# Performance work log

Hardware: AMD Instinct MI355X
Metric: run time of the kernel (lower is better)

Reference implementation:

```python
import jax, jax.numpy as jnp
import numpy as np

B, S, D_MODEL = 8, 1024, 1024
N_HEADS, N_KV_HEADS, HEAD_DIM = 16, 8, 64
ROPE_THETA = 10000.0
LN_EPS = 1e-12


def setup_inputs() -> dict:
    key = jax.random.key(0)
    ks = jax.random.split(key, 6)
    sc = 0.02
    return {
        "hidden_states": jax.random.normal(ks[0], (B, S, D_MODEL), jnp.float32),
        "Wq": jax.random.normal(ks[1], (D_MODEL, N_HEADS * HEAD_DIM), jnp.float32) * sc,
        "bq": jnp.zeros((N_HEADS * HEAD_DIM,), jnp.float32),
        "Wk": jax.random.normal(ks[2], (D_MODEL, N_KV_HEADS * HEAD_DIM), jnp.float32) * sc,
        "bk": jnp.zeros((N_KV_HEADS * HEAD_DIM,), jnp.float32),
        "Wv": jax.random.normal(ks[3], (D_MODEL, N_KV_HEADS * HEAD_DIM), jnp.float32) * sc,
        "bv": jnp.zeros((N_KV_HEADS * HEAD_DIM,), jnp.float32),
        "Wo": jax.random.normal(ks[4], (N_HEADS * HEAD_DIM, D_MODEL), jnp.float32) * sc,
        "bo": jnp.zeros((D_MODEL,), jnp.float32),
        "ln_gamma": jnp.ones((D_MODEL,), jnp.float32),
        "ln_beta": jnp.zeros((D_MODEL,), jnp.float32),
    }


def _rope_tables(seq_len, dim, dtype):
    # lucidrains RotaryEmbedding: inv_freq over even indices, interleaved pairs
    inv_freq = 1.0 / (ROPE_THETA ** (jnp.arange(0, dim, 2, dtype=jnp.float32) / dim))
    angles = jnp.arange(seq_len, dtype=jnp.float32)[:, None] * inv_freq[None, :]  # [S, dim/2]
    return jnp.cos(angles).astype(dtype), jnp.sin(angles).astype(dtype)


def _apply_rope(x, cos, sin):
    # x: [B, S, H, D]; rotate interleaved pairs (x0,x1),(x2,x3),...
    x1 = x[..., 0::2]
    x2 = x[..., 1::2]
    c = cos[None, :, None, :]
    s = sin[None, :, None, :]
    y1 = x1 * c - x2 * s
    y2 = x1 * s + x2 * c
    return jnp.stack([y1, y2], axis=-1).reshape(x.shape)


def reference(hidden_states, Wq, bq, Wk, bk, Wv, bv, Wo, bo, ln_gamma, ln_beta):
    b, s, _ = hidden_states.shape
    q = (hidden_states @ Wq + bq).reshape(b, s, N_HEADS, HEAD_DIM)
    k = (hidden_states @ Wk + bk).reshape(b, s, N_KV_HEADS, HEAD_DIM)
    v = (hidden_states @ Wv + bv).reshape(b, s, N_KV_HEADS, HEAD_DIM)

    cos, sin = _rope_tables(s, HEAD_DIM, hidden_states.dtype)
    q = _apply_rope(q, cos, sin)
    k = _apply_rope(k, cos, sin)

    # GQA: repeat_interleave kv heads to match query heads (factor 2)
    rep = N_HEADS // N_KV_HEADS
    k = jnp.repeat(k, rep, axis=2)  # [B, S, H, D]
    v = jnp.repeat(v, rep, axis=2)

    scale = 1.0 / jnp.sqrt(jnp.asarray(HEAD_DIM, hidden_states.dtype))
    scores = jnp.einsum('bqhd,bkhd->bhqk', q * scale, k)  # [B, H, S, S]
    probs = jax.nn.softmax(scores, axis=-1)
    attn = jnp.einsum('bhqk,bkhd->bqhd', probs, v).reshape(b, s, N_HEADS * HEAD_DIM)

    out = attn @ Wo + bo
    resid = out + hidden_states
    mu = jnp.mean(resid, axis=-1, keepdims=True)
    var = jnp.mean(jnp.square(resid - mu), axis=-1, keepdims=True)
    normed = (resid - mu) * jax.lax.rsqrt(var + LN_EPS)
    return normed * ln_gamma + ln_beta
```

## Files before the change

kernel.cpp:

```cpp
#include <hip/hip_runtime.h>
#include <math.h>
#include <stdint.h>

typedef unsigned short u16;
typedef __bf16 bf16x8 __attribute__((ext_vector_type(8)));
typedef float f32x4 __attribute__((ext_vector_type(4)));

typedef const __attribute__((address_space(1))) void gv_t;
typedef __attribute__((address_space(3))) void lv_t;

__device__ __forceinline__ u16 f2bf(float f) {
    unsigned u = __builtin_bit_cast(unsigned, f);
    return (u16)((u + 0x7FFFu + ((u >> 16) & 1u)) >> 16);
}
__device__ __forceinline__ float bf2f(u16 h) {
    return __builtin_bit_cast(float, (unsigned)h << 16);
}
__device__ __forceinline__ void gll16(const void* g, void* l) {
    __builtin_amdgcn_global_load_lds((gv_t*)(uintptr_t)g,
                                     (lv_t*)(unsigned)(uintptr_t)l, 16, 0, 0);
}

__global__ __launch_bounds__(256) void cvt_bf16_kernel(
    const float* __restrict__ in, u16* __restrict__ out, int n4)
{
    int i = blockIdx.x * 256 + threadIdx.x;
    if (i >= n4) return;
    float4 f = ((const float4*)in)[i];
    ushort4 o = make_ushort4(f2bf(f.x), f2bf(f.y), f2bf(f.z), f2bf(f.w));
    ((ushort4*)out)[i] = o;
}

__global__ __launch_bounds__(256) void cvt_t4_kernel(
    const float* __restrict__ w0, const float* __restrict__ w1,
    const float* __restrict__ w2, const float* __restrict__ w3,
    u16* __restrict__ o0, u16* __restrict__ o1,
    u16* __restrict__ o2, u16* __restrict__ o3)
{
    __shared__ u16 t[64][65];
    const float* in; u16* out; int N;
    switch (blockIdx.z) {
        case 0: in = w0; out = o0; N = 1024; break;
        case 1: in = w1; out = o1; N = 512;  break;
        case 2: in = w2; out = o2; N = 512;  break;
        default: in = w3; out = o3; N = 1024; break;
    }
    int kb = blockIdx.y * 64, nb = blockIdx.x * 64;
    if (nb >= N) return;
    int tid = threadIdx.x;
#pragma unroll
    for (int c = 0; c < 16; ++c) {
        int id = c * 256 + tid;
        int r = id >> 6, n = id & 63;
        t[n][r] = f2bf(in[(size_t)(kb + r) * N + nb + n]);
    }
    __syncthreads();
#pragma unroll
    for (int c = 0; c < 16; ++c) {
        int id = c * 256 + tid;
        int r = id >> 6, n = id & 63;
        out[(size_t)(nb + r) * 1024 + kb + n] = t[r][n];
    }
}

template<int MODE, int NBX>
__device__ __forceinline__ void gemm_body(
    const u16* __restrict__ A, const u16* __restrict__ Bt,
    const float* __restrict__ b0, const float* __restrict__ b1,
    const float* __restrict__ b2,
    const float* __restrict__ resid, float* __restrict__ Cf,
    u16* __restrict__ Qo, u16* __restrict__ Ko, u16* __restrict__ Vto,
    int N, int K)
{
    __shared__ __align__(16) u16 Asl[2][128 * 64];
    __shared__ __align__(16) u16 Bsl[2][128 * 64];
    const int tid = threadIdx.x, lane = tid & 63, w = tid >> 6;
    const int quad = lane >> 4, l16 = lane & 15;
    const int id = blockIdx.x;
    const int chunk = (NBX * 64) >> 3;
    const int nid = (id & 7) * chunk + (id >> 3);
    const int bx = nid & (NBX - 1), by = nid / NBX;
    const int bm = by * 128, bn = bx * 128;
    const int wm = (w >> 1) * 64, wn = (w & 1) * 64;

    f32x4 acc[4][4] = {};

    const int dr = lane >> 3;
    const int dcs = (((lane & 7) ^ dr) << 3);
    const u16* Ag = &A[(size_t)(bm + w * 32 + dr) * K + dcs];
    const u16* Bg = &Bt[(size_t)(bn + w * 32 + dr) * K + dcs];

    const int sw = l16 & 7;

    const int NT = K >> 6;
#pragma unroll
    for (int c = 0; c < 4; ++c) {
        gll16(Ag + (size_t)(c * 8) * K, &Asl[0][(w * 32 + c * 8) * 64]);
        gll16(Bg + (size_t)(c * 8) * K, &Bsl[0][(w * 32 + c * 8) * 64]);
    }
    for (int t = 0; t < NT; ++t) {
        const int cur = t & 1;
        __syncthreads();
        if (t < NT - 1) {
            const int k0 = (t + 1) * 64;
#pragma unroll
            for (int c = 0; c < 4; ++c) {
                gll16(Ag + (size_t)(c * 8) * K + k0, &Asl[cur ^ 1][(w * 32 + c * 8) * 64]);
                gll16(Bg + (size_t)(c * 8) * K + k0, &Bsl[cur ^ 1][(w * 32 + c * 8) * 64]);
            }
        }
        bf16x8 af[4][2], bfr[4][2];
#pragma unroll
        for (int i = 0; i < 4; ++i)
#pragma unroll
            for (int ks = 0; ks < 2; ++ks)
                af[i][ks] = *(const bf16x8*)&Asl[cur][(wm + i * 16 + l16) * 64 + (((ks * 4 + quad) ^ sw) << 3)];
#pragma unroll
        for (int j = 0; j < 4; ++j)
#pragma unroll
            for (int ks = 0; ks < 2; ++ks)
                bfr[j][ks] = *(const bf16x8*)&Bsl[cur][(wn + j * 16 + l16) * 64 + (((ks * 4 + quad) ^ sw) << 3)];
#pragma unroll
        for (int i = 0; i < 4; ++i)
#pragma unroll
            for (int j = 0; j < 4; ++j)
#pragma unroll
                for (int ks = 0; ks < 2; ++ks)
                    acc[i][j] = __builtin_amdgcn_mfma_f32_16x16x32_bf16(af[i][ks], bfr[j][ks], acc[i][j], 0, 0, 0);
    }

#pragma unroll
    for (int j = 0; j < 4; ++j) {
        int col = bn + wn + j * 16 + l16;
        if (MODE == 1) {
            float bb = b0[col];
#pragma unroll
            for (int i = 0; i < 4; ++i) {
                int row0 = bm + wm + i * 16 + quad * 4;
#pragma unroll
                for (int r = 0; r < 4; ++r) {
                    size_t off = (size_t)(row0 + r) * N + col;
                    Cf[off] = acc[i][j][r] + bb + resid[off];
                }
            }
        } else if (col < 1024) {
            float bb = b0[col];
#pragma unroll
            for (int i = 0; i < 4; ++i) {
                int row0 = bm + wm + i * 16 + quad * 4;
#pragma unroll
                for (int r = 0; r < 4; ++r)
                    Qo[(size_t)(row0 + r) * 1024 + col] = f2bf(acc[i][j][r] + bb);
            }
        } else if (col < 1536) {
            int c2 = col - 1024;
            float bb = b1[c2];
#pragma unroll
            for (int i = 0; i < 4; ++i) {
                int row0 = bm + wm + i * 16 + quad * 4;
#pragma unroll
                for (int r = 0; r < 4; ++r)
                    Ko[(size_t)(row0 + r) * 512 + c2] = f2bf(acc[i][j][r] + bb);
            }
        } else {
            int c2 = col - 1536, kvh = c2 >> 6, d = c2 & 63;
            float bb = b2[c2];
#pragma unroll
            for (int i = 0; i < 4; ++i) {
                int row0 = bm + wm + i * 16 + quad * 4;
                int b = row0 >> 10, s = row0 & 1023;
                ushort4 o4;
                o4.x = f2bf(acc[i][j][0] + bb);
                o4.y = f2bf(acc[i][j][1] + bb);
                o4.z = f2bf(acc[i][j][2] + bb);
                o4.w = f2bf(acc[i][j][3] + bb);
                *(ushort4*)&Vto[(size_t)((b * 8 + kvh) * 64 + d) * 1024 + s] = o4;
            }
        }
    }
}

__global__ __launch_bounds__(256) void gemm_qkv(
    const u16* __restrict__ A, const u16* __restrict__ Bt,
    const float* __restrict__ b0, const float* __restrict__ b1,
    const float* __restrict__ b2,
    u16* __restrict__ Qo, u16* __restrict__ Ko, u16* __restrict__ Vto)
{
    gemm_body<0, 16>(A, Bt, b0, b1, b2, nullptr, nullptr, Qo, Ko, Vto, 2048, 1024);
}

__global__ __launch_bounds__(256) void gemm_out(
    const u16* __restrict__ A, const u16* __restrict__ Bt,
    const float* __restrict__ b0,
    const float* __restrict__ resid, float* __restrict__ Cf)
{
    gemm_body<1, 8>(A, Bt, b0, nullptr, nullptr, resid, Cf,
                    nullptr, nullptr, nullptr, 1024, 1024);
}

__global__ __launch_bounds__(256) void rope_bf16_kernel(
    u16* __restrict__ x, int shift, int stride, int total)
{
    int idx = blockIdx.x * 256 + threadIdx.x;
    if (idx >= total) return;
    int j = idx & 31;
    int h = (idx >> 5) & ((1 << shift) - 1);
    int row = idx >> (5 + shift);
    int pos = row & 1023;
    float inv = exp2f((float)j * -0.4152410118609203f);
    float sn, cs;
    sincosf((float)pos * inv, &sn, &cs);
    unsigned* p = (unsigned*)&x[(size_t)row * stride + h * 64 + (j << 1)];
    unsigned u = *p;
    float x1 = bf2f((u16)(u & 0xffff)), x2 = bf2f((u16)(u >> 16));
    float y1 = x1 * cs - x2 * sn, y2 = x1 * sn + x2 * cs;
    *p = (unsigned)f2bf(y1) | ((unsigned)f2bf(y2) << 16);
}

__global__ __launch_bounds__(256, 4) void attn_mfma(
    const u16* __restrict__ Q, const u16* __restrict__ K,
    const u16* __restrict__ Vt, u16* __restrict__ O)
{
    __shared__ __align__(16) u16 Ks[2][64 * 64];
    __shared__ __align__(16) u16 Vts[2][64 * 64];
    __shared__ __align__(16) u16 Ps[64][40];

    const int tid = threadIdx.x, lane = tid & 63, w = tid >> 6;
    const int quad = lane >> 4, l16 = lane & 15;
    const int id = blockIdx.x;
    const int nid = (id & 7) * 128 + (id >> 3);
    const int qt = nid & 7, h = (nid >> 3) & 15, b = nid >> 7;
    const int kvh = h >> 1;
    const size_t qrow0 = (size_t)b * 1024 + qt * 128;
    const size_t krow0 = (size_t)b * 1024;
    const u16* Vg = Vt + (size_t)((b * 8 + kvh) * 64) * 1024;

    const int dr = lane >> 3;
    const int dcs = (((lane & 7) ^ dr) << 3);
    const u16* Kg0 = &K[(krow0 + w * 16 + dr) * 512 + kvh * 64 + dcs];
    const u16* Vg0 = &Vg[(size_t)(w * 16 + dr) * 1024 + dcs];
    const int sw = l16 & 7;
    const float C1 = 0.18033688011112043f;

#pragma unroll
    for (int c = 0; c < 2; ++c) {
        gll16(Kg0 + (size_t)(c * 8) * 512, &Ks[0][(w * 16 + c * 8) * 64]);
        gll16(Vg0 + (size_t)(c * 8) * 1024, &Vts[0][(w * 16 + c * 8) * 64]);
    }

    bf16x8 qf[2][2];
#pragma unroll
    for (int qg = 0; qg < 2; ++qg) {
        int qrow = w * 32 + qg * 16 + l16;
        float fpos = (float)(qt * 128 + qrow);
#pragma unroll
        for (int ks = 0; ks < 2; ++ks) {
            uint4 qraw = *(const uint4*)&Q[(qrow0 + qrow) * 1024 + h * 64 + ks * 32 + quad * 8];
            unsigned o_[4];
#pragma unroll
            for (int t = 0; t < 4; ++t) {
                int j = ks * 16 + quad * 4 + t;
                float inv = exp2f((float)j * -0.4152410118609203f);
                float sn_, cs_;
                sincosf(fpos * inv, &sn_, &cs_);
                cs_ *= C1; sn_ *= C1;
                unsigned u = (&qraw.x)[t];
                float x1 = bf2f((u16)(u & 0xffff)), x2 = bf2f((u16)(u >> 16));
                float y1 = x1 * cs_ - x2 * sn_, y2 = x1 * sn_ + x2 * cs_;
                o_[t] = (unsigned)f2bf(y1) | ((unsigned)f2bf(y2) << 16);
            }
            qf[qg][ks] = __builtin_bit_cast(bf16x8, make_uint4(o_[0], o_[1], o_[2], o_[3]));
        }
    }

    f32x4 acc_o[2][4] = {};
    f32x4 lsum[2] = {};
    const bf16x8 ones = __builtin_bit_cast(bf16x8,
        make_uint4(0x3F803F80u, 0x3F803F80u, 0x3F803F80u, 0x3F803F80u));

    for (int kt = 0; kt < 16; ++kt) {
        const int cur = kt & 1;
        __syncthreads();

        if (kt < 15) {
#pragma unroll
            for (int c = 0; c < 2; ++c) {
                gll16(Kg0 + (size_t)((kt + 1) * 64 + c * 8) * 512,
                      &Ks[cur ^ 1][(w * 16 + c * 8) * 64]);
                gll16(Vg0 + (size_t)(c * 8) * 1024 + (kt + 1) * 64,
                      &Vts[cur ^ 1][(w * 16 + c * 8) * 64]);
            }
        }

        f32x4 s[2][4] = {};
        __builtin_amdgcn_s_setprio(1);
#pragma unroll
        for (int ks = 0; ks < 2; ++ks) {
#pragma unroll
            for (int nt = 0; nt < 4; ++nt) {
                bf16x8 ak = *(const bf16x8*)&Ks[cur][(nt * 16 + l16) * 64 + (((ks * 4 + quad) ^ sw) << 3)];
                s[0][nt] = __builtin_amdgcn_mfma_f32_16x16x32_bf16(ak, qf[0][ks], s[0][nt], 0, 0, 0);
                s[1][nt] = __builtin_amdgcn_mfma_f32_16x16x32_bf16(ak, qf[1][ks], s[1][nt], 0, 0, 0);
            }
        }
        __builtin_amdgcn_s_setprio(0);

#pragma unroll
        for (int kc = 0; kc < 2; ++kc) {
            bf16x8 av[4];
#pragma unroll
            for (int nt = 0; nt < 4; ++nt)
                av[nt] = *(const bf16x8*)&Vts[cur][(nt * 16 + l16) * 64 + (((kc * 4 + quad) ^ sw) << 3)];
#pragma unroll
            for (int qg = 0; qg < 2; ++qg) {
#pragma unroll
                for (int ntl = 0; ntl < 2; ++ntl) {
                    int nt = kc * 2 + ntl;
                    float p0 = __builtin_amdgcn_exp2f(s[qg][nt][0]);
                    float p1 = __builtin_amdgcn_exp2f(s[qg][nt][1]);
                    unsigned pk0 = __builtin_amdgcn_perm(
                        __builtin_bit_cast(unsigned, p1),
                        __builtin_bit_cast(unsigned, p0), 0x07060302u);
                    float p2 = __builtin_amdgcn_exp2f(s[qg][nt][2]);
                    float p3 = __builtin_amdgcn_exp2f(s[qg][nt][3]);
                    unsigned pk1 = __builtin_amdgcn_perm(
                        __builtin_bit_cast(unsigned, p3),
                        __builtin_bit_cast(unsigned, p2), 0x07060302u);
                    *(uint2*)&Ps[w * 16 + l16][ntl * 16 + quad * 4] = make_uint2(pk0, pk1);
                }
                bf16x8 bp = *(const bf16x8*)&Ps[w * 16 + l16][quad * 8];
                __builtin_amdgcn_s_setprio(1);
                lsum[qg] = __builtin_amdgcn_mfma_f32_16x16x32_bf16(ones, bp, lsum[qg], 0, 0, 0);
#pragma unroll
                for (int nt = 0; nt < 4; ++nt)
                    acc_o[qg][nt] = __builtin_amdgcn_mfma_f32_16x16x32_bf16(av[nt], bp, acc_o[qg][nt], 0, 0, 0);
                __builtin_amdgcn_s_setprio(0);
            }
        }
    }

#pragma unroll
    for (int qg = 0; qg < 2; ++qg) {
        float rl = 1.0f / lsum[qg][0];
        size_t orow = (qrow0 + w * 32 + qg * 16 + l16) * 1024 + h * 64;
#pragma unroll
        for (int nt = 0; nt < 4; ++nt) {
            ushort4 o4;
            o4.x = f2bf(acc_o[qg][nt][0] * rl);
            o4.y = f2bf(acc_o[qg][nt][1] * rl);
            o4.z = f2bf(acc_o[qg][nt][2] * rl);
            o4.w = f2bf(acc_o[qg][nt][3] * rl);
            *(ushort4*)&O[orow + nt * 16 + quad * 4] = o4;
        }
    }
}

__global__ __launch_bounds__(256) void ln_kernel(float* __restrict__ io,
    const float* __restrict__ gamma, const float* __restrict__ beta)
{
    int row = blockIdx.x;
    int tid = threadIdx.x;
    float* p = io + (size_t)row * 1024;
    float4 x = *reinterpret_cast<const float4*>(&p[tid << 2]);
    float s = x.x + x.y + x.z + x.w;
    float ss = fmaf(x.x, x.x, fmaf(x.y, x.y, fmaf(x.z, x.z, x.w * x.w)));
#pragma unroll
    for (int off = 32; off > 0; off >>= 1) {
        s  += __shfl_down(s, off);
        ss += __shfl_down(ss, off);
    }
    __shared__ float rs[4], rss[4];
    int lane = tid & 63, wid = tid >> 6;
    if (lane == 0) { rs[wid] = s; rss[wid] = ss; }
    __syncthreads();
    float S = rs[0] + rs[1] + rs[2] + rs[3];
    float SS = rss[0] + rss[1] + rss[2] + rss[3];
    float mu = S * (1.0f / 1024.0f);
    float var = SS * (1.0f / 1024.0f) - mu * mu;
    float rstd = rsqrtf(var + 1e-12f);
    float4 g = *reinterpret_cast<const float4*>(&gamma[tid << 2]);
    float4 be = *reinterpret_cast<const float4*>(&beta[tid << 2]);
    float4 o;
    o.x = (x.x - mu) * rstd * g.x + be.x;
    o.y = (x.y - mu) * rstd * g.y + be.y;
    o.z = (x.z - mu) * rstd * g.z + be.z;
    o.w = (x.w - mu) * rstd * g.w + be.w;
    *reinterpret_cast<float4*>(&p[tid << 2]) = o;
}

extern "C" void kernel_launch(void* const* d_in, const int* in_sizes, int n_in,
                              void* d_out, int out_size, void* d_ws, size_t ws_size,
                              hipStream_t stream)
{
    (void)in_sizes; (void)n_in; (void)out_size; (void)ws_size;
    const float* hidden = (const float*)d_in[0];
    const float* Wq = (const float*)d_in[1];
    const float* bq = (const float*)d_in[2];
    const float* Wk = (const float*)d_in[3];
    const float* bk = (const float*)d_in[4];
    const float* Wv = (const float*)d_in[5];
    const float* bv = (const float*)d_in[6];
    const float* Wo = (const float*)d_in[7];
    const float* bo = (const float*)d_in[8];
    const float* g  = (const float*)d_in[9];
    const float* be = (const float*)d_in[10];
    float* out = (float*)d_out;

    u16* hb  = (u16*)d_ws;
    u16* Wqt = hb  + (size_t)8192 * 1024;
    u16* Wkt = Wqt + (size_t)1024 * 1024;
    u16* Wvt = Wkt + (size_t)512 * 1024;
    u16* Wot = Wvt + (size_t)512 * 1024;
    u16* Qb  = Wot + (size_t)1024 * 1024;
    u16* Kb  = Qb  + (size_t)8192 * 1024;
    u16* Vtb = Kb  + (size_t)8192 * 512;

    cvt_bf16_kernel<<<8192, 256, 0, stream>>>(hidden, hb, 8192 * 1024 / 4);
    cvt_t4_kernel<<<dim3(16, 16, 4), 256, 0, stream>>>(Wq, Wk, Wv, Wo, Wqt, Wkt, Wvt, Wot);

    gemm_qkv<<<dim3(1024), 256, 0, stream>>>(hb, Wqt, bq, bk, bv, Qb, Kb, Vtb);

    rope_bf16_kernel<<<8192, 256, 0, stream>>>(Kb, 3, 512, 8192 * 8 * 32);

    attn_mfma<<<dim3(1024), 256, 0, stream>>>(Qb, Kb, Vtb, Qb);

    gemm_out<<<dim3(512), 256, 0, stream>>>(Qb, Wot, bo, hidden, out);

    ln_kernel<<<8192, 256, 0, stream>>>(out, g, be);
}
```

Before: 235.4 us.

## Fuse conversion kernels, vectorize K rope, keep P in registers for PV MFMA

Merges the hidden-state bf16 conversion and the weight transpose-conversion into a single launch, saving one kernel launch. The K rope kernel now has each thread handle four rotation pairs through 16-byte loads and stores. In attention, the softmax probabilities no longer round-trip through LDS. The packed exp values are used directly as the MFMA B operand, and the V fragments are reloaded with a matching permuted k-ordering so the products stay consistent. This removes LDS traffic but relies on the permutation of the reduction index being correct.

```diff
diff --git a/kernel.cpp b/kernel.cpp
--- a/kernel.cpp
+++ b/kernel.cpp
@@ -21,33 +21,33 @@
                                      (lv_t*)(unsigned)(uintptr_t)l, 16, 0, 0);
 }
 
-__global__ __launch_bounds__(256) void cvt_bf16_kernel(
-    const float* __restrict__ in, u16* __restrict__ out, int n4)
-{
-    int i = blockIdx.x * 256 + threadIdx.x;
-    if (i >= n4) return;
-    float4 f = ((const float4*)in)[i];
-    ushort4 o = make_ushort4(f2bf(f.x), f2bf(f.y), f2bf(f.z), f2bf(f.w));
-    ((ushort4*)out)[i] = o;
-}
-
-__global__ __launch_bounds__(256) void cvt_t4_kernel(
+__global__ __launch_bounds__(256) void cvt_all_kernel(
+    const float* __restrict__ hidden, u16* __restrict__ hb,
     const float* __restrict__ w0, const float* __restrict__ w1,
     const float* __restrict__ w2, const float* __restrict__ w3,
     u16* __restrict__ o0, u16* __restrict__ o1,
     u16* __restrict__ o2, u16* __restrict__ o3)
 {
     __shared__ u16 t[64][65];
+    int bid = blockIdx.x, tid = threadIdx.x;
+    if (bid < 8192) {
+        int i = bid * 256 + tid;
+        float4 f = ((const float4*)hidden)[i];
+        ushort4 o = make_ushort4(f2bf(f.x), f2bf(f.y), f2bf(f.z), f2bf(f.w));
+        ((ushort4*)hb)[i] = o;
+        return;
+    }
+    int id2 = bid - 8192;
+    int bz = id2 >> 8, by = (id2 >> 4) & 15, bx = id2 & 15;
     const float* in; u16* out; int N;
-    switch (blockIdx.z) {
+    switch (bz) {
         case 0: in = w0; out = o0; N = 1024; break;
         case 1: in = w1; out = o1; N = 512;  break;
         case 2: in = w2; out = o2; N = 512;  break;
         default: in = w3; out = o3; N = 1024; break;
     }
-    int kb = blockIdx.y * 64, nb = blockIdx.x * 64;
+    int kb = by * 64, nb = bx * 64;
     if (nb >= N) return;
-    int tid = threadIdx.x;
 #pragma unroll
     for (int c = 0; c < 16; ++c) {
         int id = c * 256 + tid;
@@ -198,23 +198,27 @@
                     nullptr, nullptr, nullptr, 1024, 1024);
 }
 
-__global__ __launch_bounds__(256) void rope_bf16_kernel(
-    u16* __restrict__ x, int shift, int stride, int total)
+__global__ __launch_bounds__(256) void rope_bf16_kernel(u16* __restrict__ x)
 {
     int idx = blockIdx.x * 256 + threadIdx.x;
-    if (idx >= total) return;
-    int j = idx & 31;
-    int h = (idx >> 5) & ((1 << shift) - 1);
-    int row = idx >> (5 + shift);
-    int pos = row & 1023;
-    float inv = exp2f((float)j * -0.4152410118609203f);
-    float sn, cs;
-    sincosf((float)pos * inv, &sn, &cs);
-    unsigned* p = (unsigned*)&x[(size_t)row * stride + h * 64 + (j << 1)];
-    unsigned u = *p;
-    float x1 = bf2f((u16)(u & 0xffff)), x2 = bf2f((u16)(u >> 16));
-    float y1 = x1 * cs - x2 * sn, y2 = x1 * sn + x2 * cs;
-    *p = (unsigned)f2bf(y1) | ((unsigned)f2bf(y2) << 16);
+    int jg = idx & 7;
+    int h = (idx >> 3) & 7;
+    int row = idx >> 6;
+    float fpos = (float)(row & 1023);
+    uint4 u4 = *(uint4*)&x[(size_t)row * 512 + h * 64 + jg * 8];
+    unsigned* uw = &u4.x;
+#pragma unroll
+    for (int t = 0; t < 4; ++t) {
+        int j = jg * 4 + t;
+        float inv = exp2f((float)j * -0.4152410118609203f);
+        float sn, cs;
+        sincosf(fpos * inv, &sn, &cs);
+        unsigned u = uw[t];
+        float x1 = bf2f((u16)(u & 0xffff)), x2 = bf2f((u16)(u >> 16));
+        float y1 = x1 * cs - x2 * sn, y2 = x1 * sn + x2 * cs;
+        uw[t] = (unsigned)f2bf(y1) | ((unsigned)f2bf(y2) << 16);
+    }
+    *(uint4*)&x[(size_t)row * 512 + h * 64 + jg * 8] = u4;
 }
 
 __global__ __launch_bounds__(256, 4) void attn_mfma(
@@ -223,7 +227,6 @@
 {
     __shared__ __align__(16) u16 Ks[2][64 * 64];
     __shared__ __align__(16) u16 Vts[2][64 * 64];
-    __shared__ __align__(16) u16 Ps[64][40];
 
     const int tid = threadIdx.x, lane = tid & 63, w = tid >> 6;
     const int quad = lane >> 4, l16 = lane & 15;
@@ -307,33 +310,41 @@
 
 #pragma unroll
         for (int kc = 0; kc < 2; ++kc) {
-            bf16x8 av[4];
-#pragma unroll
-            for (int nt = 0; nt < 4; ++nt)
-                av[nt] = *(const bf16x8*)&Vts[cur][(nt * 16 + l16) * 64 + (((kc * 4 + quad) ^ sw) << 3)];
+            uint2 vlo[4], vhi[4];
+            const int pcl = ((kc * 4 + (quad >> 1)) ^ sw) * 8 + (quad & 1) * 4;
+            const int pch = ((kc * 4 + 2 + (quad >> 1)) ^ sw) * 8 + (quad & 1) * 4;
+#pragma unroll
+            for (int nt = 0; nt < 4; ++nt) {
+                vlo[nt] = *(const uint2*)&Vts[cur][(nt * 16 + l16) * 64 + pcl];
+                vhi[nt] = *(const uint2*)&Vts[cur][(nt * 16 + l16) * 64 + pch];
+            }
 #pragma unroll
             for (int qg = 0; qg < 2; ++qg) {
+                unsigned pk[4];
 #pragma unroll
                 for (int ntl = 0; ntl < 2; ++ntl) {
                     int nt = kc * 2 + ntl;
                     float p0 = __builtin_amdgcn_exp2f(s[qg][nt][0]);
                     float p1 = __builtin_amdgcn_exp2f(s[qg][nt][1]);
-                    unsigned pk0 = __builtin_amdgcn_perm(
+                    pk[ntl * 2 + 0] = __builtin_amdgcn_perm(
                         __builtin_bit_cast(unsigned, p1),
                         __builtin_bit_cast(unsigned, p0), 0x07060302u);
                     float p2 = __builtin_amdgcn_exp2f(s[qg][nt][2]);
                     float p3 = __builtin_amdgcn_exp2f(s[qg][nt][3]);
-                    unsigned pk1 = __builtin_amdgcn_perm(
+                    pk[ntl * 2 + 1] = __builtin_amdgcn_perm(
                         __builtin_bit_cast(unsigned, p3),
                         __builtin_bit_cast(unsigned, p2), 0x07060302u);
-                    *(uint2*)&Ps[w * 16 + l16][ntl * 16 + quad * 4] = make_uint2(pk0, pk1);
                 }
-                bf16x8 bp = *(const bf16x8*)&Ps[w * 16 + l16][quad * 8];
+                bf16x8 bp = __builtin_bit_cast(bf16x8,
+                    make_uint4(pk[0], pk[1], pk[2], pk[3]));
                 __builtin_amdgcn_s_setprio(1);
                 lsum[qg] = __builtin_amdgcn_mfma_f32_16x16x32_bf16(ones, bp, lsum[qg], 0, 0, 0);
 #pragma unroll
-                for (int nt = 0; nt < 4; ++nt)
-                    acc_o[qg][nt] = __builtin_amdgcn_mfma_f32_16x16x32_bf16(av[nt], bp, acc_o[qg][nt], 0, 0, 0);
+                for (int nt = 0; nt < 4; ++nt) {
+                    bf16x8 av = __builtin_bit_cast(bf16x8,
+                        make_uint4(vlo[nt].x, vlo[nt].y, vhi[nt].x, vhi[nt].y));
+                    acc_o[qg][nt] = __builtin_amdgcn_mfma_f32_16x16x32_bf16(av, bp, acc_o[qg][nt], 0, 0, 0);
+                }
                 __builtin_amdgcn_s_setprio(0);
             }
         }
@@ -415,12 +426,12 @@
     u16* Kb  = Qb  + (size_t)8192 * 1024;
     u16* Vtb = Kb  + (size_t)8192 * 512;
 
-    cvt_bf16_kernel<<<8192, 256, 0, stream>>>(hidden, hb, 8192 * 1024 / 4);
-    cvt_t4_kernel<<<dim3(16, 16, 4), 256, 0, stream>>>(Wq, Wk, Wv, Wo, Wqt, Wkt, Wvt, Wot);
+    cvt_all_kernel<<<9216, 256, 0, stream>>>(hidden, hb, Wq, Wk, Wv, Wo,
+                                             Wqt, Wkt, Wvt, Wot);
 
     gemm_qkv<<<dim3(1024), 256, 0, stream>>>(hb, Wqt, bq, bk, bv, Qb, Kb, Vtb);
 
-    rope_bf16_kernel<<<8192, 256, 0, stream>>>(Kb, 3, 512, 8192 * 8 * 32);
+    rope_bf16_kernel<<<2048, 256, 0, stream>>>(Kb);
 
     attn_mfma<<<dim3(1024), 256, 0, stream>>>(Qb, Kb, Vtb, Qb);
 
```

Result: no change. 235.0 us (-0.2%).

## Fuse K rope into QKV GEMM epilogue and merge conversion kernels

Applied to the files above, without the earlier changes.

Applies the rotary embedding to K inside the QKV GEMM epilogue. Each lane exchanges its pair partner's value with a lane shuffle and computes sin/cos inline, which removes the separate rope kernel and its extra read/write pass over K. The hidden-state cast and the weight transpose-cast kernels are also merged into one launch with a flattened grid to save one launch. In exchange the GEMM epilogue does extra transcendental work per K element and carries extra register pressure.

```diff
diff --git a/kernel.cpp b/kernel.cpp
--- a/kernel.cpp
+++ b/kernel.cpp
@@ -21,33 +21,33 @@
                                      (lv_t*)(unsigned)(uintptr_t)l, 16, 0, 0);
 }
 
-__global__ __launch_bounds__(256) void cvt_bf16_kernel(
-    const float* __restrict__ in, u16* __restrict__ out, int n4)
-{
-    int i = blockIdx.x * 256 + threadIdx.x;
-    if (i >= n4) return;
-    float4 f = ((const float4*)in)[i];
-    ushort4 o = make_ushort4(f2bf(f.x), f2bf(f.y), f2bf(f.z), f2bf(f.w));
-    ((ushort4*)out)[i] = o;
-}
-
-__global__ __launch_bounds__(256) void cvt_t4_kernel(
+__global__ __launch_bounds__(256) void cvt_all_kernel(
+    const float* __restrict__ hidden, u16* __restrict__ hb,
     const float* __restrict__ w0, const float* __restrict__ w1,
     const float* __restrict__ w2, const float* __restrict__ w3,
     u16* __restrict__ o0, u16* __restrict__ o1,
     u16* __restrict__ o2, u16* __restrict__ o3)
 {
     __shared__ u16 t[64][65];
+    int bid = blockIdx.x, tid = threadIdx.x;
+    if (bid < 8192) {
+        int i = bid * 256 + tid;
+        float4 f = ((const float4*)hidden)[i];
+        ushort4 o = make_ushort4(f2bf(f.x), f2bf(f.y), f2bf(f.z), f2bf(f.w));
+        ((ushort4*)hb)[i] = o;
+        return;
+    }
+    int id2 = bid - 8192;
+    int bz = id2 >> 8, by = (id2 >> 4) & 15, bx = id2 & 15;
     const float* in; u16* out; int N;
-    switch (blockIdx.z) {
+    switch (bz) {
         case 0: in = w0; out = o0; N = 1024; break;
         case 1: in = w1; out = o1; N = 512;  break;
         case 2: in = w2; out = o2; N = 512;  break;
         default: in = w3; out = o3; N = 1024; break;
     }
-    int kb = blockIdx.y * 64, nb = blockIdx.x * 64;
+    int kb = by * 64, nb = bx * 64;
     if (nb >= N) return;
-    int tid = threadIdx.x;
 #pragma unroll
     for (int c = 0; c < 16; ++c) {
         int id = c * 256 + tid;
@@ -155,12 +155,20 @@
         } else if (col < 1536) {
             int c2 = col - 1024;
             float bb = b1[c2];
+            int jj = (c2 & 63) >> 1;
+            float inv = exp2f((float)jj * -0.4152410118609203f);
+            float sgn = (l16 & 1) ? 1.0f : -1.0f;
 #pragma unroll
             for (int i = 0; i < 4; ++i) {
                 int row0 = bm + wm + i * 16 + quad * 4;
 #pragma unroll
-                for (int r = 0; r < 4; ++r)
-                    Ko[(size_t)(row0 + r) * 512 + c2] = f2bf(acc[i][j][r] + bb);
+                for (int r = 0; r < 4; ++r) {
+                    float v = acc[i][j][r] + bb;
+                    float o = __shfl_xor(v, 1);
+                    float sn, cs;
+                    sincosf((float)((row0 + r) & 1023) * inv, &sn, &cs);
+                    Ko[(size_t)(row0 + r) * 512 + c2] = f2bf(fmaf(v, cs, sgn * (o * sn)));
+                }
             }
         } else {
             int c2 = col - 1536, kvh = c2 >> 6, d = c2 & 63;
@@ -196,25 +204,6 @@
 {
     gemm_body<1, 8>(A, Bt, b0, nullptr, nullptr, resid, Cf,
                     nullptr, nullptr, nullptr, 1024, 1024);
-}
-
-__global__ __launch_bounds__(256) void rope_bf16_kernel(
-    u16* __restrict__ x, int shift, int stride, int total)
-{
-    int idx = blockIdx.x * 256 + threadIdx.x;
-    if (idx >= total) return;
-    int j = idx & 31;
-    int h = (idx >> 5) & ((1 << shift) - 1);
-    int row = idx >> (5 + shift);
-    int pos = row & 1023;
-    float inv = exp2f((float)j * -0.4152410118609203f);
-    float sn, cs;
-    sincosf((float)pos * inv, &sn, &cs);
-    unsigned* p = (unsigned*)&x[(size_t)row * stride + h * 64 + (j << 1)];
-    unsigned u = *p;
-    float x1 = bf2f((u16)(u & 0xffff)), x2 = bf2f((u16)(u >> 16));
-    float y1 = x1 * cs - x2 * sn, y2 = x1 * sn + x2 * cs;
-    *p = (unsigned)f2bf(y1) | ((unsigned)f2bf(y2) << 16);
 }
 
 __global__ __launch_bounds__(256, 4) void attn_mfma(
@@ -415,13 +404,11 @@
     u16* Kb  = Qb  + (size_t)8192 * 1024;
     u16* Vtb = Kb  + (size_t)8192 * 512;
 
-    cvt_bf16_kernel<<<8192, 256, 0, stream>>>(hidden, hb, 8192 * 1024 / 4);
-    cvt_t4_kernel<<<dim3(16, 16, 4), 256, 0, stream>>>(Wq, Wk, Wv, Wo, Wqt, Wkt, Wvt, Wot);
+    cvt_all_kernel<<<9216, 256, 0, stream>>>(hidden, hb, Wq, Wk, Wv, Wo,
+                                             Wqt, Wkt, Wvt, Wot);
 
     gemm_qkv<<<dim3(1024), 256, 0, stream>>>(hb, Wqt, bq, bk, bv, Qb, Kb, Vtb);
 
-    rope_bf16_kernel<<<8192, 256, 0, stream>>>(Kb, 3, 512, 8192 * 8 * 32);
-
     attn_mfma<<<dim3(1024), 256, 0, stream>>>(Qb, Kb, Vtb, Qb);
 
     gemm_out<<<dim3(512), 256, 0, stream>>>(Qb, Wot, bo, hidden, out);
```

After: 470.7 us. 2x slower.
